# Kernel optimization log

Measured on AMD Instinct MI355X. Metric: run time of the kernel, lower is better.

Reference implementation:

```python
import jax, jax.numpy as jnp
import numpy as np

B, L = 8, 16384
H = 64          # num_channel
N2 = 32         # s4_hidden_size // 2 complex conjugate-pair modes
DEPTH = 4       # model_depth
NLAYERS = 1 + DEPTH  # number of DSSM layers
EPS = 1e-5


def setup_inputs() -> dict:
    key = jax.random.key(0)
    ks = jax.random.split(key, 12)
    x = jax.random.normal(ks[0], (B, L), dtype=jnp.float32)
    # input linear 1 -> H
    w_in = jax.random.normal(ks[1], (H,), dtype=jnp.float32)
    b_in = jax.random.normal(ks[2], (H,), dtype=jnp.float32) * 0.1
    # hidden linears H -> H
    w_mid = jax.random.normal(ks[3], (DEPTH, H, H), dtype=jnp.float32) / np.sqrt(H)
    b_mid = jax.random.normal(ks[4], (DEPTH, H), dtype=jnp.float32) * 0.1
    # output linear H -> 1
    w_out = jax.random.normal(ks[5], (H,), dtype=jnp.float32) / np.sqrt(H)
    b_out = jax.random.normal(ks[6], (), dtype=jnp.float32) * 0.1
    # S4D / DSSM parameters (stacked over the 5 SSM layers)
    log_dt = (jax.random.uniform(ks[7], (NLAYERS, H), dtype=jnp.float32)
              * (np.log(0.1) - np.log(0.001)) + np.log(0.001))
    log_A_real = jnp.log(0.5 * jnp.ones((NLAYERS, H, N2), dtype=jnp.float32))
    A_imag = jnp.pi * jnp.broadcast_to(jnp.arange(N2, dtype=jnp.float32), (NLAYERS, H, N2))
    C_re = jax.random.normal(ks[8], (NLAYERS, H, N2), dtype=jnp.float32)
    C_im = jax.random.normal(ks[9], (NLAYERS, H, N2), dtype=jnp.float32)
    D = jax.random.normal(ks[10], (NLAYERS, H), dtype=jnp.float32)
    return {"x": x, "w_in": w_in, "b_in": b_in, "w_mid": w_mid, "b_mid": b_mid,
            "w_out": w_out, "b_out": b_out, "log_dt": log_dt,
            "log_A_real": log_A_real, "A_imag": A_imag,
            "C_re": C_re, "C_im": C_im, "D": D}


def _dssm(u, log_dt, log_A_real, A_imag, C_re, C_im, D):
    # u: [B, H, L]; diagonal SSM applied as FFT convolution (S4D ZOH kernel)
    Lq = u.shape[-1]
    dt = jnp.exp(log_dt)                      # [H]
    A = -jnp.exp(log_A_real) + 1j * A_imag    # [H, N2]
    dtA = A * dt[:, None]                     # [H, N2]
    C_eff = (C_re + 1j * C_im) * (jnp.exp(dtA) - 1.0) / A
    # Vandermonde: exp(dtA * l) for l in [0, L)
    V = jnp.exp(dtA[:, :, None] * jnp.arange(Lq, dtype=jnp.float32))  # [H, N2, L]
    k = 2.0 * jnp.einsum('hn,hnl->hl', C_eff, V).real                # [H, L]
    uf = jnp.fft.rfft(u, n=2 * Lq)
    kf = jnp.fft.rfft(k, n=2 * Lq)
    y = jnp.fft.irfft(uf * kf, n=2 * Lq)[..., :Lq]
    return y + u * D[:, None]


def reference(x, w_in, b_in, w_mid, b_mid, w_out, b_out,
              log_dt, log_A_real, A_imag, C_re, C_im, D):
    # side chain: Abs -> Decibel -> Linear(1,H) -> tanh -> [DSSM -> tanh] ...
    s = 20.0 * jnp.log10(jnp.abs(x) + EPS)            # [B, L]
    h = jnp.tanh(s[..., None] * w_in + b_in)          # [B, L, H]
    h = jnp.tanh(_dssm(h.transpose(0, 2, 1), log_dt[0], log_A_real[0],
                       A_imag[0], C_re[0], C_im[0], D[0]).transpose(0, 2, 1))
    for i in range(DEPTH):
        h = jnp.tanh(jnp.einsum('blh,oh->blo', h, w_mid[i]) + b_mid[i])
        j = i + 1
        h = jnp.tanh(_dssm(h.transpose(0, 2, 1), log_dt[j], log_A_real[j],
                           A_imag[j], C_re[j], C_im[j], D[j]).transpose(0, 2, 1))
    g = jnp.einsum('blh,h->bl', h, w_out) + b_out      # [B, L]
    g = jnp.power(10.0, g / 20.0)                      # Amplitude (dB -> linear)
    return x * g
```

## Files before the change

### kernel.cpp

```cpp
#include <hip/hip_runtime.h>
#include <math.h>

#define Bq 8
#define Lq 16384
#define Hq 64
#define N2q 32
#define NLAYERSq 5

typedef _Float16 f16x8 __attribute__((ext_vector_type(8)));
typedef _Float16 f16x4 __attribute__((ext_vector_type(4)));
typedef float    f32x4 __attribute__((ext_vector_type(4)));

#define MFMA16F(a, b, c) __builtin_amdgcn_mfma_f32_16x16x32_f16(a, b, c, 0, 0, 0)

#define UT_OFF    0
#define SF_OFF    49152
#define SMEM_SZ   81920
#define YST_OFF   0
#define SF(row, c) ((row) * 128 + ((c) ^ ((row) & 31)))

#define WT_OFF_B   0
#define WP_OFF_B   163840
#define A2_OFF_B   (163840 + 5242880)
#define U_OFF_B    (163840 + 5242880 + 15728640)

__device__ __forceinline__ float fast_tanh(float y) {
    float e = __expf(2.0f * y);
    return 1.0f - 2.0f * __builtin_amdgcn_rcpf(e + 1.0f);
}

__global__ __launch_bounds__(256)
void k_prep(const float* __restrict__ log_dt, const float* __restrict__ log_A_real,
            const float* __restrict__ A_imag, const float* __restrict__ C_re,
            const float* __restrict__ C_im, const float* __restrict__ Dvec,
            float* __restrict__ wT_tab, _Float16* __restrict__ Wp,
            _Float16* __restrict__ A2) {
    __shared__ float Pr[129][33], Pi[129][33];
    __shared__ float cre[32], cim[32], Kv[128];
    __shared__ double sdAr[32], sdAi[32];
    const int ph = blockIdx.x;
    const int tid = threadIdx.x;

    if (tid < 32) {
        int n = tid;
        int pidx = ph * N2q + n;
        double dt  = exp((double)log_dt[ph]);
        double aRe = -exp((double)log_A_real[pidx]);
        double aIm = (double)A_imag[pidx];
        double dAr = aRe * dt, dAi = aIm * dt;
        sdAr[n] = dAr; sdAi[n] = dAi;
        double er  = exp(dAr);
        double wre = er * cos(dAi), wim = er * sin(dAi);
        double Er = wre - 1.0, Ei = wim;
        double inv = 1.0 / (aRe * aRe + aIm * aIm);
        double Fr = (Er * aRe + Ei * aIm) * inv;
        double Fi = (Ei * aRe - Er * aIm) * inv;
        double Cr = (double)C_re[pidx], Ci = (double)C_im[pidx];
        cre[n] = (float)(2.0 * (Cr * Fr - Ci * Fi));
        cim[n] = (float)(2.0 * (Cr * Fi + Ci * Fr));
        double qr = wre, qi = wim;
        #pragma unroll
        for (int s = 0; s < 7; s++) {
            double nr = qr * qr - qi * qi;
            qi = 2.0 * qr * qi; qr = nr;
        }
        float wTr = (float)qr, wTi = (float)qi;
        #pragma unroll
        for (int s = 0; s < 3; s++) {
            double nr = qr * qr - qi * qi;
            qi = 2.0 * qr * qi; qr = nr;
        }
        float* wt = wT_tab + ph * 128 + n * 4;
        wt[0] = wTr; wt[1] = wTi; wt[2] = (float)qr; wt[3] = (float)qi;
    }
    __syncthreads();

    const double TWO_PI  = 6.2831853071795864769;
    const double INV_2PI = 0.15915494309189533577;
    for (int e = tid; e < 129 * 32; e += 256) {
        int j = e >> 5, n = e & 31;
        double phd = (double)j * sdAi[n];
        double r   = fma(-TWO_PI, nearbyint(phd * INV_2PI), phd);
        float  mag = __expf((float)((double)j * sdAr[n]));
        float  rf  = (float)r;
        Pr[j][n] = mag * cosf(rf);
        Pi[j][n] = mag * sinf(rf);
    }
    __syncthreads();

    if (tid < 128) {
        int d = tid;
        float s = 0.f;
        #pragma unroll 8
        for (int n = 0; n < 32; n++)
            s += cre[n] * Pr[d][n] - cim[n] * Pi[d][n];
        if (d == 0) s += Dvec[ph];
        Kv[d] = s;
    }
    __syncthreads();

    _Float16* wpb = Wp + (size_t)ph * 8192;
    for (int e = tid; e < 8192; e += 256) {
        int kk = e >> 7, l = e & 127;
        float v = (kk < 32) ? Pr[127 - l][kk] : Pi[127 - l][kk - 32];
        wpb[e] = (_Float16)v;
    }
    _Float16* a2b = A2 + (size_t)ph * 24576;
    for (int e = tid; e < 24576; e += 256) {
        int m = e / 192, k = e - m * 192;
        float v;
        if (k < 128) {
            v = (k <= m) ? Kv[m - k] : 0.f;
        } else {
            int kk = k - 128, n2 = kk & 31;
            float pr = Pr[m + 1][n2], pi2 = Pi[m + 1][n2];
            v = (kk < 32) ? (cre[n2] * pr - cim[n2] * pi2)
                          : -(cre[n2] * pi2 + cim[n2] * pr);
        }
        a2b[e] = (_Float16)v;
    }
}

__global__ __launch_bounds__(512, 4)
void k_scan(const float* __restrict__ x, _Float16* __restrict__ u16,
            const _Float16* __restrict__ Wp_all, const _Float16* __restrict__ A2_all,
            const float* __restrict__ wT_all, int layer,
            const float* __restrict__ w_in, const float* __restrict__ b_in) {
    extern __shared__ char smem[];
    _Float16* UT = (_Float16*)(smem + UT_OFF);
    float*    Sf = (float*)(smem + SF_OFF);
    float*   yst = (float*)(smem + YST_OFF);

    const int bh = blockIdx.x;
    const int h  = bh & 63;
    const int tid = threadIdx.x;
    const int lane = tid & 63;
    const int wave = tid >> 6;
    const int ph = layer * 64 + h;
    const _Float16* Wp = Wp_all + (size_t)ph * 8192;
    const _Float16* A2 = A2_all + (size_t)ph * 24576;
    const float* wT4 = wT_all + ph * 128;
    _Float16* uu = u16 + ((size_t)bh << 14);

    const int rA = lane & 15;
    const int qA = lane >> 4;

    if (layer == 0) {
        const float* xb = x + ((size_t)(bh >> 6) << 14);
        const float wi = w_in[h], bi = b_in[h];
        for (int it = 0; it < 4; ++it) {
            int flat8 = (it * 512 + tid) * 8;
            int n = flat8 >> 7, k = flat8 & 127;
            float4 a = *(const float4*)(xb + flat8);
            float4 b = *(const float4*)(xb + flat8 + 4);
            float f[8] = {a.x, a.y, a.z, a.w, b.x, b.y, b.z, b.w};
            f16x8 hv;
            #pragma unroll
            for (int j = 0; j < 8; j++) {
                float s = 6.0205999132796239f * __log2f(fabsf(f[j]) + 1e-5f);
                hv[j] = (_Float16)fast_tanh(fmaf(s, wi, bi));
            }
            int kb = (k * 2) ^ ((n & 7) << 4);
            *(f16x8*)((char*)UT + n * 384 + kb) = hv;
        }
    } else {
        for (int it = 0; it < 4; ++it) {
            int flat8 = (it * 512 + tid) * 8;
            int n = flat8 >> 7, k = flat8 & 127;
            f16x8 hv = *(const f16x8*)(uu + flat8);
            int kb = (k * 2) ^ ((n & 7) << 4);
            *(f16x8*)((char*)UT + n * 384 + kb) = hv;
        }
    }
    __syncthreads();

    {
        f32x4 acc1[4];
        #pragma unroll
        for (int nt = 0; nt < 4; nt++) acc1[nt] = (f32x4){0.f, 0.f, 0.f, 0.f};
        const int mt1 = wave & 3;
        const int nh  = (wave >> 2) * 4;
        for (int ks = 0; ks < 4; ks++) {
            f16x8 af = *(const f16x8*)(Wp + (mt1 * 16 + rA) * 128 + ks * 32 + qA * 8);
            #pragma unroll
            for (int nt = 0; nt < 4; nt++) {
                int n = (nh + nt) * 16 + rA;
                int kb = (ks * 64 + qA * 16) ^ ((n & 7) << 4);
                f16x8 bv = *(const f16x8*)((char*)UT + n * 384 + kb);
                acc1[nt] = MFMA16F(af, bv, acc1[nt]);
            }
        }
        #pragma unroll
        for (int nt = 0; nt < 4; nt++) {
            int c = (nh + nt) * 16 + rA;
            #pragma unroll
            for (int r = 0; r < 4; r++)
                Sf[SF(mt1 * 16 + qA * 4 + r, c)] = acc1[nt][r];
        }
    }
    __syncthreads();

    {
        const int sn = tid >> 4;
        const int ss = tid & 15;
        const float wTr = wT4[sn * 4 + 0], wTi = wT4[sn * 4 + 1];
        float fr[8], fi[8];
        #pragma unroll
        for (int i = 0; i < 8; i++) {
            fr[i] = Sf[SF(sn,      ss * 8 + i)];
            fi[i] = Sf[SF(sn + 32, ss * 8 + i)];
        }
        float Tr = 0.f, Ti = 0.f;
        #pragma unroll
        for (int i = 0; i < 8; i++) {
            float nTr = fmaf(wTr, Tr, fmaf(-wTi, Ti, fr[i]));
            Ti = fmaf(wTr, Ti, fmaf(wTi, Tr, fi[i]));
            Tr = nTr;
        }
        float gr = wT4[sn * 4 + 2], gi = wT4[sn * 4 + 3];
        #pragma unroll
        for (int s = 0; s < 4; s++) {
            float pr = __shfl_up(Tr, 1 << s, 16);
            float pi = __shfl_up(Ti, 1 << s, 16);
            if (ss >= (1 << s)) {
                Tr = fmaf(gr, pr, fmaf(-gi, pi, Tr));
                Ti = fmaf(gr, pi, fmaf(gi, pr, Ti));
            }
            float ngr = fmaf(gr, gr, -gi * gi);
            gi = 2.f * gr * gi; gr = ngr;
        }
        float Er_ = __shfl_up(Tr, 1, 16);
        float Ei_ = __shfl_up(Ti, 1, 16);
        if (ss == 0) { Er_ = 0.f; Ei_ = 0.f; }
        float Gr = Er_, Gi = Ei_;
        #pragma unroll
        for (int i = 0; i < 8; i++) {
            Sf[SF(sn,      ss * 8 + i)] = Gr;
            Sf[SF(sn + 32, ss * 8 + i)] = Gi;
            float nGr = fmaf(wTr, Gr, fmaf(-wTi, Gi, fr[i]));
            Gi = fmaf(wTr, Gi, fmaf(wTi, Gr, fi[i]));
            Gr = nGr;
        }
    }
    __syncthreads();

    for (int e = tid; e < 8192; e += 512) {
        int kk = e >> 7, c = e & 127;
        float v = Sf[SF(kk, c)];
        int kb = (256 + kk * 2) ^ ((c & 7) << 4);
        *(_Float16*)((char*)UT + c * 384 + kb) = (_Float16)v;
    }
    __syncthreads();

    f32x4 acc[8];
    #pragma unroll
    for (int nt = 0; nt < 8; nt++) acc[nt] = (f32x4){0.f, 0.f, 0.f, 0.f};
    for (int ks = 0; ks < 6; ks++) {
        f16x8 a0 = *(const f16x8*)(A2 + (wave * 16 + rA) * 192 + ks * 32 + qA * 8);
        #pragma unroll
        for (int nt = 0; nt < 8; nt++) {
            int n = nt * 16 + rA;
            int kb = (ks * 64 + qA * 16) ^ ((n & 7) << 4);
            f16x8 bv = *(const f16x8*)((char*)UT + n * 384 + kb);
            acc[nt] = MFMA16F(a0, bv, acc[nt]);
        }
    }
    __syncthreads();

    {
        int m_base = wave * 16 + qA * 4;
        #pragma unroll
        for (int nt = 0; nt < 8; nt++) {
            int c = nt * 16 + rA;
            float4 o;
            o.x = fast_tanh(acc[nt][0]);
            o.y = fast_tanh(acc[nt][1]);
            o.z = fast_tanh(acc[nt][2]);
            o.w = fast_tanh(acc[nt][3]);
            *(float4*)(yst + c * 132 + m_base) = o;
        }
    }
    __syncthreads();
    for (int e = tid; e < 2048; e += 512) {
        int c = e >> 4, l8 = e & 15;
        float4 v0 = *(const float4*)(yst + c * 132 + l8 * 8);
        float4 v1 = *(const float4*)(yst + c * 132 + l8 * 8 + 4);
        f16x8 hv;
        hv[0] = (_Float16)v0.x; hv[1] = (_Float16)v0.y;
        hv[2] = (_Float16)v0.z; hv[3] = (_Float16)v0.w;
        hv[4] = (_Float16)v1.x; hv[5] = (_Float16)v1.y;
        hv[6] = (_Float16)v1.z; hv[7] = (_Float16)v1.w;
        *(f16x8*)(uu + c * 128 + l8 * 8) = hv;
    }
}

__global__ __launch_bounds__(256)
void k_linear(_Float16* __restrict__ uio, const float* __restrict__ W,
              const float* __restrict__ bias) {
    __shared__ float Wt[64][68];
    __shared__ float Ut[64][64];
    const int b  = blockIdx.y;
    const int l0 = blockIdx.x * 64;
    const int tid = threadIdx.x;

    for (int idx = tid; idx < 4096; idx += 256) {
        int o = idx >> 6, hh = idx & 63;
        Wt[hh][o] = W[idx];
        Ut[o][hh] = (float)uio[(((size_t)(b << 6) | o) << 14) + l0 + hh];
    }
    __syncthreads();

    float acc[4][4];
    #pragma unroll
    for (int j = 0; j < 4; j++)
        #pragma unroll
        for (int k = 0; k < 4; k++) acc[j][k] = 0.f;

    const int og = (tid >> 4) << 2;
    const int lg = (tid & 15) << 2;

    #pragma unroll 4
    for (int hh = 0; hh < 64; ++hh) {
        float4 wv = *(const float4*)&Wt[hh][og];
        float4 uv = *(const float4*)&Ut[hh][lg];
        acc[0][0] = fmaf(wv.x, uv.x, acc[0][0]); acc[0][1] = fmaf(wv.x, uv.y, acc[0][1]);
        acc[0][2] = fmaf(wv.x, uv.z, acc[0][2]); acc[0][3] = fmaf(wv.x, uv.w, acc[0][3]);
        acc[1][0] = fmaf(wv.y, uv.x, acc[1][0]); acc[1][1] = fmaf(wv.y, uv.y, acc[1][1]);
        acc[1][2] = fmaf(wv.y, uv.z, acc[1][2]); acc[1][3] = fmaf(wv.y, uv.w, acc[1][3]);
        acc[2][0] = fmaf(wv.z, uv.x, acc[2][0]); acc[2][1] = fmaf(wv.z, uv.y, acc[2][1]);
        acc[2][2] = fmaf(wv.z, uv.z, acc[2][2]); acc[2][3] = fmaf(wv.z, uv.w, acc[2][3]);
        acc[3][0] = fmaf(wv.w, uv.x, acc[3][0]); acc[3][1] = fmaf(wv.w, uv.y, acc[3][1]);
        acc[3][2] = fmaf(wv.w, uv.z, acc[3][2]); acc[3][3] = fmaf(wv.w, uv.w, acc[3][3]);
    }

    #pragma unroll
    for (int j = 0; j < 4; j++) {
        float bo = bias[og + j];
        f16x4 o4;
        o4[0] = (_Float16)fast_tanh(acc[j][0] + bo);
        o4[1] = (_Float16)fast_tanh(acc[j][1] + bo);
        o4[2] = (_Float16)fast_tanh(acc[j][2] + bo);
        o4[3] = (_Float16)fast_tanh(acc[j][3] + bo);
        *(f16x4*)&uio[(((size_t)(b << 6) | (og + j)) << 14) + l0 + lg] = o4;
    }
}

__global__ __launch_bounds__(256)
void k_out(const _Float16* __restrict__ u16, const float* __restrict__ x,
           const float* __restrict__ w_out, const float* __restrict__ b_out,
           float* __restrict__ out) {
    int idx = blockIdx.x * 256 + threadIdx.x;
    int b = idx >> 14;
    int l = idx & (Lq - 1);
    const _Float16* up = u16 + ((size_t)b << 20) + l;
    float acc = 0.f;
    #pragma unroll 8
    for (int hh = 0; hh < 64; ++hh)
        acc = fmaf(w_out[hh], (float)up[(size_t)hh << 14], acc);
    float g = acc + b_out[0];
    out[idx] = x[idx] * exp2f(g * 0.16609640474436812f);
}

extern "C" void kernel_launch(void* const* d_in, const int* in_sizes, int n_in,
                              void* d_out, int out_size, void* d_ws, size_t ws_size,
                              hipStream_t stream) {
    const float* x          = (const float*)d_in[0];
    const float* w_in       = (const float*)d_in[1];
    const float* b_in       = (const float*)d_in[2];
    const float* w_mid      = (const float*)d_in[3];
    const float* b_mid      = (const float*)d_in[4];
    const float* w_out      = (const float*)d_in[5];
    const float* b_out      = (const float*)d_in[6];
    const float* log_dt     = (const float*)d_in[7];
    const float* log_A_real = (const float*)d_in[8];
    const float* A_imag     = (const float*)d_in[9];
    const float* C_re       = (const float*)d_in[10];
    const float* C_im       = (const float*)d_in[11];
    const float* Dv         = (const float*)d_in[12];

    char* ws = (char*)d_ws;
    float*     wT_tab = (float*)(ws + WT_OFF_B);
    _Float16*  Wp     = (_Float16*)(ws + WP_OFF_B);
    _Float16*  A2     = (_Float16*)(ws + A2_OFF_B);
    _Float16*  u16    = (_Float16*)(ws + U_OFF_B);
    float* out = (float*)d_out;

    hipFuncSetAttribute((const void*)k_scan,
                        hipFuncAttributeMaxDynamicSharedMemorySize, SMEM_SZ);

    k_prep<<<NLAYERSq * Hq, 256, 0, stream>>>(log_dt, log_A_real, A_imag,
                                              C_re, C_im, Dv, wT_tab, Wp, A2);
    for (int layer = 0; layer < NLAYERSq; layer++) {
        if (layer > 0)
            k_linear<<<dim3(Lq / 64, Bq), 256, 0, stream>>>(
                u16, w_mid + (size_t)(layer - 1) * Hq * Hq, b_mid + (size_t)(layer - 1) * Hq);
        k_scan<<<Bq * Hq, 512, SMEM_SZ, stream>>>(x, u16, Wp, A2, wT_tab, layer,
                                                  w_in, b_in);
    }
    k_out<<<(Bq * Lq) / 256, 256, 0, stream>>>(u16, x, w_out, b_out, out);
}
```

Baseline: 214.8 us.

## Run hidden linear layers on fp16 MFMA with swizzled LDS tiles

Rewrites the per-layer 64x64 channel-mixing linear kernel to use 16x16x32 fp16 MFMA instructions instead of scalar fp32 FMAs. Weights are converted to fp16 once in the prep kernel, activation tiles are widened to 256 positions per block, loaded with 16-byte vector loads into an XOR-swizzled LDS layout, and the output is staged through LDS so global stores are coalesced. This targets the scalar-FMA compute and the narrow 2-byte global accesses of the old kernel, at the cost of fp16 weight rounding and fewer, larger blocks.

```diff
diff --git a/kernel.cpp b/kernel.cpp
--- a/kernel.cpp
+++ b/kernel.cpp
@@ -22,7 +22,8 @@
 #define WT_OFF_B   0
 #define WP_OFF_B   163840
 #define A2_OFF_B   (163840 + 5242880)
-#define U_OFF_B    (163840 + 5242880 + 15728640)
+#define W16_OFF_B  (163840 + 5242880 + 15728640)
+#define U_OFF_B    (163840 + 5242880 + 15728640 + 32768)
 
 __device__ __forceinline__ float fast_tanh(float y) {
     float e = __expf(2.0f * y);
@@ -33,13 +34,19 @@
 void k_prep(const float* __restrict__ log_dt, const float* __restrict__ log_A_real,
             const float* __restrict__ A_imag, const float* __restrict__ C_re,
             const float* __restrict__ C_im, const float* __restrict__ Dvec,
+            const float* __restrict__ w_mid,
             float* __restrict__ wT_tab, _Float16* __restrict__ Wp,
-            _Float16* __restrict__ A2) {
+            _Float16* __restrict__ A2, _Float16* __restrict__ W16) {
     __shared__ float Pr[129][33], Pi[129][33];
     __shared__ float cre[32], cim[32], Kv[128];
     __shared__ double sdAr[32], sdAi[32];
     const int ph = blockIdx.x;
     const int tid = threadIdx.x;
+
+    if (ph < 256 && tid < 64) {
+        int e = ph * 64 + tid;
+        W16[e] = (_Float16)w_mid[e];
+    }
 
     if (tid < 32) {
         int n = tid;
@@ -294,54 +301,75 @@
     }
 }
 
-__global__ __launch_bounds__(256)
-void k_linear(_Float16* __restrict__ uio, const float* __restrict__ W,
+__global__ __launch_bounds__(256, 4)
+void k_linear(_Float16* __restrict__ uio, const _Float16* __restrict__ W16,
               const float* __restrict__ bias) {
-    __shared__ float Wt[64][68];
-    __shared__ float Ut[64][64];
-    const int b  = blockIdx.y;
-    const int l0 = blockIdx.x * 64;
+    __shared__ __align__(16) char lmem[33792];
+    _Float16* Ul  = (_Float16*)lmem;
+    _Float16* yst = (_Float16*)lmem;
+
+    const int b   = blockIdx.y;
+    const int l0  = blockIdx.x * 256;
     const int tid = threadIdx.x;
-
-    for (int idx = tid; idx < 4096; idx += 256) {
-        int o = idx >> 6, hh = idx & 63;
-        Wt[hh][o] = W[idx];
-        Ut[o][hh] = (float)uio[(((size_t)(b << 6) | o) << 14) + l0 + hh];
-    }
-    __syncthreads();
-
-    float acc[4][4];
+    const int lane = tid & 63;
+    const int wave = tid >> 6;
+    const int rA = lane & 15;
+    const int qA = lane >> 4;
+
+    _Float16* ub = uio + ((size_t)b << 20) + l0;
+
+    for (int it = 0; it < 4; ++it) {
+        int g  = it * 256 + tid;
+        int hp = g >> 5;
+        int l8 = g & 31;
+        f16x8 v0 = *(const f16x8*)(ub + (size_t)(hp * 2)     * Lq + l8 * 8);
+        f16x8 v1 = *(const f16x8*)(ub + (size_t)(hp * 2 + 1) * Lq + l8 * 8);
+        const unsigned short* p0 = (const unsigned short*)&v0;
+        const unsigned short* p1 = (const unsigned short*)&v1;
+        int sw = (l8 & 7) << 4;
+        #pragma unroll
+        for (int j = 0; j < 8; j++) {
+            unsigned int pk = (unsigned int)p0[j] | ((unsigned int)p1[j] << 16);
+            *(unsigned int*)((char*)Ul + (l8 * 8 + j) * 128 + ((hp * 4) ^ sw)) = pk;
+        }
+    }
+    __syncthreads();
+
+    f32x4 acc[16];
     #pragma unroll
-    for (int j = 0; j < 4; j++)
-        #pragma unroll
-        for (int k = 0; k < 4; k++) acc[j][k] = 0.f;
-
-    const int og = (tid >> 4) << 2;
-    const int lg = (tid & 15) << 2;
-
-    #pragma unroll 4
-    for (int hh = 0; hh < 64; ++hh) {
-        float4 wv = *(const float4*)&Wt[hh][og];
-        float4 uv = *(const float4*)&Ut[hh][lg];
-        acc[0][0] = fmaf(wv.x, uv.x, acc[0][0]); acc[0][1] = fmaf(wv.x, uv.y, acc[0][1]);
-        acc[0][2] = fmaf(wv.x, uv.z, acc[0][2]); acc[0][3] = fmaf(wv.x, uv.w, acc[0][3]);
-        acc[1][0] = fmaf(wv.y, uv.x, acc[1][0]); acc[1][1] = fmaf(wv.y, uv.y, acc[1][1]);
-        acc[1][2] = fmaf(wv.y, uv.z, acc[1][2]); acc[1][3] = fmaf(wv.y, uv.w, acc[1][3]);
-        acc[2][0] = fmaf(wv.z, uv.x, acc[2][0]); acc[2][1] = fmaf(wv.z, uv.y, acc[2][1]);
-        acc[2][2] = fmaf(wv.z, uv.z, acc[2][2]); acc[2][3] = fmaf(wv.z, uv.w, acc[2][3]);
-        acc[3][0] = fmaf(wv.w, uv.x, acc[3][0]); acc[3][1] = fmaf(wv.w, uv.y, acc[3][1]);
-        acc[3][2] = fmaf(wv.w, uv.z, acc[3][2]); acc[3][3] = fmaf(wv.w, uv.w, acc[3][3]);
-    }
-
+    for (int nt = 0; nt < 16; nt++) acc[nt] = (f32x4){0.f, 0.f, 0.f, 0.f};
+    const _Float16* Wrow = W16 + (wave * 16 + rA) * 64;
     #pragma unroll
-    for (int j = 0; j < 4; j++) {
-        float bo = bias[og + j];
-        f16x4 o4;
-        o4[0] = (_Float16)fast_tanh(acc[j][0] + bo);
-        o4[1] = (_Float16)fast_tanh(acc[j][1] + bo);
-        o4[2] = (_Float16)fast_tanh(acc[j][2] + bo);
-        o4[3] = (_Float16)fast_tanh(acc[j][3] + bo);
-        *(f16x4*)&uio[(((size_t)(b << 6) | (og + j)) << 14) + l0 + lg] = o4;
+    for (int kf = 0; kf < 2; kf++) {
+        f16x8 af = *(const f16x8*)(Wrow + kf * 32 + qA * 8);
+        #pragma unroll
+        for (int nt = 0; nt < 16; nt++) {
+            int n = nt * 16 + rA;
+            int sw = ((n >> 3) & 7) << 4;
+            f16x8 bv = *(const f16x8*)((char*)Ul + n * 128 + ((kf * 64 + qA * 16) ^ sw));
+            acc[nt] = MFMA16F(af, bv, acc[nt]);
+        }
+    }
+    __syncthreads();
+
+    {
+        int ob = wave * 16 + qA * 4;
+        float bo0 = bias[ob], bo1 = bias[ob + 1], bo2 = bias[ob + 2], bo3 = bias[ob + 3];
+        #pragma unroll
+        for (int nt = 0; nt < 16; nt++) {
+            int l = nt * 16 + rA;
+            yst[(ob + 0) * 264 + l] = (_Float16)fast_tanh(acc[nt][0] + bo0);
+            yst[(ob + 1) * 264 + l] = (_Float16)fast_tanh(acc[nt][1] + bo1);
+            yst[(ob + 2) * 264 + l] = (_Float16)fast_tanh(acc[nt][2] + bo2);
+            yst[(ob + 3) * 264 + l] = (_Float16)fast_tanh(acc[nt][3] + bo3);
+        }
+    }
+    __syncthreads();
+    for (int it = 0; it < 8; ++it) {
+        int e = it * 256 + tid;
+        int o = e >> 5, l8 = e & 31;
+        f16x8 hv = *(const f16x8*)(yst + o * 264 + l8 * 8);
+        *(f16x8*)(ub + (size_t)o * Lq + l8 * 8) = hv;
     }
 }
 
@@ -382,6 +410,7 @@
     float*     wT_tab = (float*)(ws + WT_OFF_B);
     _Float16*  Wp     = (_Float16*)(ws + WP_OFF_B);
     _Float16*  A2     = (_Float16*)(ws + A2_OFF_B);
+    _Float16*  W16    = (_Float16*)(ws + W16_OFF_B);
     _Float16*  u16    = (_Float16*)(ws + U_OFF_B);
     float* out = (float*)d_out;
 
@@ -389,11 +418,12 @@
                         hipFuncAttributeMaxDynamicSharedMemorySize, SMEM_SZ);
 
     k_prep<<<NLAYERSq * Hq, 256, 0, stream>>>(log_dt, log_A_real, A_imag,
-                                              C_re, C_im, Dv, wT_tab, Wp, A2);
+                                              C_re, C_im, Dv, w_mid,
+                                              wT_tab, Wp, A2, W16);
     for (int layer = 0; layer < NLAYERSq; layer++) {
         if (layer > 0)
-            k_linear<<<dim3(Lq / 64, Bq), 256, 0, stream>>>(
-                u16, w_mid + (size_t)(layer - 1) * Hq * Hq, b_mid + (size_t)(layer - 1) * Hq);
+            k_linear<<<dim3(Lq / 256, Bq), 256, 0, stream>>>(
+                u16, W16 + (size_t)(layer - 1) * Hq * Hq, b_mid + (size_t)(layer - 1) * Hq);
         k_scan<<<Bq * Hq, 512, SMEM_SZ, stream>>>(x, u16, Wp, A2, wT_tab, layer,
                                                   w_in, b_in);
     }
```

Measured after the change: 184.3 us. 1.17x faster.
